# Optimization experiments

Measured on AMD Instinct MI355X. Metric: run time of the kernel, lower is better.

Reference implementation:

```python
import jax, jax.numpy as jnp
import numpy as np

EPS_GN = 1e-8
EPS_ATTN = 1e-8


def setup_inputs() -> dict:
    key = jax.random.key(0)
    ks = jax.random.split(key, 13)
    B, C, N = 4, 512, 2048
    s = 0.02
    return {
        "x": jax.random.normal(ks[0], (B, C, N), jnp.float32),
        "dw_w": jax.random.normal(ks[1], (C, 3), jnp.float32) * s,
        "pw_w": jax.random.normal(ks[2], (C, C), jnp.float32) * s,
        "u_w": jax.random.normal(ks[3], (2 * C, C), jnp.float32) * s,
        "u_b": jax.random.normal(ks[4], (2 * C,), jnp.float32) * s,
        "v_w": jax.random.normal(ks[5], (2 * C, C), jnp.float32) * s,
        "v_b": jax.random.normal(ks[6], (2 * C,), jnp.float32) * s,
        "h_w": jax.random.normal(ks[7], (C, C), jnp.float32) * s,
        "h_b": jax.random.normal(ks[8], (C,), jnp.float32) * s,
        "q_w": jax.random.normal(ks[9], (C, C), jnp.float32) * s,
        "k_w": jax.random.normal(ks[10], (C, C), jnp.float32) * s,
        "o_w": jax.random.normal(ks[11], (C, 2 * C), jnp.float32) * s,
        "o_b": jax.random.normal(ks[12], (C,), jnp.float32) * s,
    }


def reference(x, dw_w, pw_w, u_w, u_b, v_w, v_b, h_w, h_b, q_w, k_w, o_w, o_b):
    # x: [B, C, N]
    C = x.shape[1]
    # GroupNorm(1, C): normalize over (C, N) per sample; affine is identity-init
    # in torch but we follow the module math with default weight=1, bias=0
    mean = jnp.mean(x, axis=(1, 2), keepdims=True)
    var = jnp.var(x, axis=(1, 2), keepdims=True)
    z = (x - mean) * jax.lax.rsqrt(var + EPS_GN)

    # local depthwise conv k=3, pad=1 (cross-correlation), no bias
    zp = jnp.pad(z, ((0, 0), (0, 0), (1, 1)))
    dw = (dw_w[:, 0, None] * zp[:, :, :-2]
          + dw_w[:, 1, None] * zp[:, :, 1:-1]
          + dw_w[:, 2, None] * zp[:, :, 2:])
    # pointwise conv (no bias)
    z = z + jnp.einsum('oc,bcn->bon', pw_w, dw)

    u = jax.nn.sigmoid(jnp.einsum('oc,bcn->bon', u_w, z) + u_b[:, None])  # [B,2C,N]
    v = jnp.einsum('oc,bcn->bon', v_w, z) + v_b[:, None]                  # [B,2C,N]
    h = jnp.einsum('oc,bcn->bno', h_w, z) + h_b                           # [B,N,C]

    q = h @ q_w.T  # [B,N,C]
    k = h @ k_w.T  # [B,N,C]
    scale = 1.0 / jnp.sqrt(jnp.float32(C))

    logits = jnp.einsum('bnc,bmc->bnm', q, k) * scale
    a = jax.nn.relu(logits)
    a = a * a
    a = a / (jnp.sum(a, axis=-1, keepdims=True) + EPS_ATTN)

    av = jnp.einsum('bnm,bom->bon', a, v)  # [B,2C,N]
    y = jnp.einsum('oc,bcn->bon', o_w, u * av) + o_b[:, None]
    return x + y
```

## Files before the change

kernel.cpp:

```cpp
#include <hip/hip_runtime.h>
#include <hip/hip_bf16.h>
#include <cstdint>

typedef __bf16 bhalf;
typedef __bf16 bhalf8 __attribute__((ext_vector_type(8)));
typedef float f32x4 __attribute__((ext_vector_type(4)));

enum { EPI_Z2=0, EPI_UV=1, EPI_BIAS=2, EPI_QK=3, EPI_ATTN=4, EPI_PV=5, EPI_Y=6 };

__device__ __forceinline__ void gl_lds16(const bhalf* g, bhalf* l) {
  __builtin_amdgcn_global_load_lds(
      (const __attribute__((address_space(1))) unsigned int*)g,
      (__attribute__((address_space(3))) unsigned int*)l,
      16, 0, 0);
}
__device__ __forceinline__ void barrier_raw() { asm volatile("s_barrier" ::: "memory"); }
#define VMW(n)  asm volatile("s_waitcnt vmcnt(" #n ")" ::: "memory")
#define LGKM0() asm volatile("s_waitcnt lgkmcnt(0)" ::: "memory")


template<int EPI>
__global__ void __launch_bounds__(512, 2)
gA(const bhalf* __restrict__ A, const bhalf* __restrict__ Bw,
   void* __restrict__ Out, void* __restrict__ Out2,
   const float* __restrict__ bias, const float* __restrict__ bias2,
   int N, int K, long sA, long sB, long sO, long sAuxf, float scale)
{
  constexpr int KSL = 256*64;
  constexpr int REG = 2*KSL;
  constexpr int DBUF = 2*REG;
  __shared__ __align__(16) char lds[2*DBUF];

  const int gx = gridDim.x, gy = gridDim.y;
  const int nwg = gx*gy;
  const int flat = blockIdx.y*gx + blockIdx.x;
  const int q8 = nwg>>3, r8 = nwg&7, xcd = flat&7, o8 = flat>>3;
  const int wsw = (xcd<r8 ? xcd*(q8+1) : r8*(q8+1)+(xcd-r8)*q8) + o8;
  const int bx = wsw % gx, by = wsw / gx;
  const int m0 = by*256, n0 = bx*256;
  const int bz = blockIdx.z;

  const bhalf* Ab = A + (long)bz*sA;
  const bhalf* Bb = Bw + (long)bz*sB;

  const int tid = threadIdx.x, wid = tid>>6, lane = tid&63;
  const int lm = lane&15, kq = lane>>4;
  const int wm = wid>>2, wn = wid&3;
  const int srow = lane>>2;
  const int csw = ((lane&3) ^ ((lane>>3)&3)) * 8;
  const int kqs = kq ^ ((lm>>1)&3);

  f32x4 acc[8][4];
  #pragma unroll
  for (int i=0;i<8;i++)
    #pragma unroll
    for (int j=0;j<4;j++) acc[i][j] = f32x4{0.f,0.f,0.f,0.f};

  auto stageA = [&](int kt){
    char* base = lds + (kt&1)*DBUF;
    const int k0 = kt*64;
    #pragma unroll
    for (int h=0; h<2; h++)
      #pragma unroll
      for (int ksl=0; ksl<2; ksl++){
        bhalf* d = (bhalf*)(base + ksl*KSL + (h*128 + wid*16)*64);
        gl_lds16(Ab + (long)(m0 + h*128 + wid*16 + srow)*K + k0 + ksl*32 + csw, d);
      }
  };
  auto stageB = [&](int kt){
    char* base = lds + (kt&1)*DBUF + REG;
    const int k0 = kt*64;
    #pragma unroll
    for (int h=0; h<2; h++)
      #pragma unroll
      for (int ksl=0; ksl<2; ksl++){
        bhalf* d = (bhalf*)(base + ksl*KSL + (h*128 + wid*16)*64);
        gl_lds16(Bb + (long)(n0 + h*128 + wid*16 + srow)*K + k0 + ksl*32 + csw, d);
      }
  };

  bhalf8 af[4][2], bf[4][2];
  auto readA = [&](int kt, int ih){
    char* base = lds + (kt&1)*DBUF;
    #pragma unroll
    for (int i2=0;i2<4;i2++)
      #pragma unroll
      for (int ksl=0;ksl<2;ksl++)
        af[i2][ksl] = *(const bhalf8*)(base + ksl*KSL + (wm*128 + ih*64 + i2*16 + lm)*64 + kqs*16);
  };
  auto readB = [&](int kt, int jh){
    char* base = lds + (kt&1)*DBUF + REG;
    #pragma unroll
    for (int j2=0;j2<2;j2++)
      #pragma unroll
      for (int ksl=0;ksl<2;ksl++)
        bf[jh*2+j2][ksl] = *(const bhalf8*)(base + ksl*KSL + (wn*64 + jh*32 + j2*16 + lm)*64 + kqs*16);
  };
  auto mfma16 = [&](int ih, int jh){
    __builtin_amdgcn_s_setprio(1);
    #pragma unroll
    for (int i2=0;i2<4;i2++)
      #pragma unroll
      for (int j2=0;j2<2;j2++)
        #pragma unroll
        for (int ksl=0;ksl<2;ksl++)
          acc[ih*4+i2][jh*2+j2] = __builtin_amdgcn_mfma_f32_16x16x32_bf16(
              af[i2][ksl], bf[jh*2+j2][ksl], acc[ih*4+i2][jh*2+j2], 0,0,0);
    __builtin_amdgcn_s_setprio(0);
  };

  const int NT = K>>6;
  stageA(0); stageB(0); stageA(1);
  for (int kt=0; kt<NT; ++kt){
    if (kt==NT-1) { VMW(0); } else { VMW(4); }
    barrier_raw();
    readA(kt,0); readB(kt,0);
    if (kt+1<NT) stageB(kt+1);
    mfma16(0,0);
    barrier_raw();
    readB(kt,1);
    mfma16(0,1);
    barrier_raw();
    readA(kt,1);
    mfma16(1,0);
    barrier_raw();
    if (kt+2<NT) stageA(kt+2);
    mfma16(1,1);
  }
  barrier_raw();

  if constexpr (EPI==EPI_ATTN){
    float rs[8][4];
    #pragma unroll
    for (int i=0;i<8;i++)
      #pragma unroll
      for (int r=0;r<4;r++) rs[i][r]=0.f;
    #pragma unroll
    for (int i=0;i<8;i++){
      #pragma unroll
      for (int j=0;j<4;j++){
        const int lcol = wn*64 + j*16 + lm;
        #pragma unroll
        for (int r=0;r<4;r++){
          const int lrow = wm*128 + i*16 + kq*4 + r;
          float v = acc[i][j][r];
          v *= scale; v = fmaxf(v,0.f); v = v*v;
          rs[i][r] += v;
          const int cb = lcol*2;
          const int lb = lrow*512 + (((cb>>5) ^ ((lrow>>2)&3))<<5) + (cb&31);
          *(bhalf*)(lds + lb) = (bhalf)v;
        }
      }
    }
    float* rd = (float*)Out2;
    #pragma unroll
    for (int i=0;i<8;i++){
      const int rbase = m0 + wm*128 + i*16 + kq*4;
      #pragma unroll
      for (int r=0;r<4;r++){
        float s = rs[i][r];
        s += __shfl_xor(s,1); s += __shfl_xor(s,2);
        s += __shfl_xor(s,4); s += __shfl_xor(s,8);
        if (lm==0) atomicAdd(rd + (long)bz*sAuxf + rbase + r, s);
      }
    }
    LGKM0();
    barrier_raw();
    char* obase = (char*)Out + 2*((long)bz*sO + (long)m0*N + n0);
    const int ldb = N*2;
    #pragma unroll
    for (int it=0; it<16; ++it){
      const int g = (it*512 + tid)*16;
      const int row = g >> 9, off = g & 511;
      const int lb = row*512 + (((off>>5) ^ ((row>>2)&3))<<5) + (off&31);
      uint4 val = *(const uint4*)(lds + lb);
      *(uint4*)(obase + (long)row*ldb + off) = val;
    }
  }
  if constexpr (EPI==EPI_UV){
    const bool uh = n0 < 1024;
    const float* bv = uh ? bias : bias2;
    const int bc0 = uh ? n0 : n0-1024;
    #pragma unroll
    for (int i=0;i<8;i++){
      #pragma unroll
      for (int j=0;j<4;j++){
        const int lcol = wn*64 + j*16 + lm;
        #pragma unroll
        for (int r=0;r<4;r++){
          const int lrow = wm*128 + i*16 + kq*4 + r;
          float v = acc[i][j][r] + bv[bc0 + lcol];
          if (uh){
            v = 1.f/(1.f + __expf(-v));
            const int cb = lcol*2;
            const int lb = lrow*512 + (((cb>>5) ^ ((lrow>>2)&3))<<5) + (cb&31);
            *(bhalf*)(lds + lb) = (bhalf)v;
          } else {
            const int lb = lcol*512 + 2*(lrow ^ ((lcol&15)<<2));
            *(bhalf*)(lds + lb) = (bhalf)v;
          }
        }
      }
    }
    LGKM0();
    barrier_raw();
    if (uh){
      char* obase = (char*)Out + 2*((long)m0*1024 + n0);
      #pragma unroll
      for (int it=0; it<16; ++it){
        const int g = (it*512 + tid)*16;
        const int row = g >> 9, off = g & 511;
        const int lb = row*512 + (((off>>5) ^ ((row>>2)&3))<<5) + (off&31);
        uint4 val = *(const uint4*)(lds + lb);
        *(uint4*)(obase + (long)row*2048 + off) = val;
      }
    } else {
      char* vb = (char*)Out2 + 2*((long)(m0>>11)*1024*2048 + (long)(n0-1024)*2048 + (m0 & 2047));
      #pragma unroll
      for (int it=0; it<16; ++it){
        const int g = (it*512 + tid)*16;
        const int row = g >> 9, off = g & 511;
        const int t0 = off >> 1;
        const int s = (row&15)<<2;
        unsigned long long lo = *(const unsigned long long*)(lds + row*512 + 2*(t0^s));
        unsigned long long hi = *(const unsigned long long*)(lds + row*512 + 2*((t0+4)^s));
        char* dst = vb + (long)row*4096 + off;
        ((unsigned long long*)dst)[0] = lo;
        ((unsigned long long*)dst)[1] = hi;
      }
    }
  }
  (void)scale; (void)bias; (void)bias2; (void)N;
}

template<int EPI>
__global__ void __launch_bounds__(256, 2)
g4k(const bhalf* __restrict__ A, const bhalf* __restrict__ Bw,
    void* __restrict__ Out, void* __restrict__ Out2,
    const float* __restrict__ bias,
    const bhalf* __restrict__ auxb, const float* __restrict__ auxf,
    const float* __restrict__ xadd,
    int M, int N, int K, long sB, int rowshift)
{
  constexpr int KSL = 256*64;
  constexpr int DBUF = 2*KSL;
  __shared__ __align__(16) char lds[2*DBUF];

  const int gx = gridDim.x, gy = gridDim.y;
  const int nwg = gx*gy;
  const int flat = blockIdx.y*gx + blockIdx.x;
  const int q8 = nwg>>3, r8 = nwg&7, xcd = flat&7, o8 = flat>>3;
  const int w = (xcd<r8 ? xcd*(q8+1) : r8*(q8+1)+(xcd-r8)*q8) + o8;
  const int bx = w % gx, by = w / gx;
  const int m0 = by*128, n0 = bx*128;

  const bhalf* Bb = Bw + (rowshift ? (long)(m0>>rowshift)*sB : 0);

  const int tid = threadIdx.x;
  const int wid = tid>>6, lane = tid&63;
  const int lm = lane&15, kq = lane>>4;
  const int wm = wid>>1, wn = wid&1;
  const int srow = lane>>2;
  const int csw = ((lane&3) ^ ((lane>>3)&3))*8;
  const int kqs = kq ^ ((lm>>1)&3);

  f32x4 acc[4][4];
  #pragma unroll
  for (int i=0;i<4;i++)
    #pragma unroll
    for (int j=0;j<4;j++) acc[i][j] = f32x4{0.f,0.f,0.f,0.f};

  auto stage = [&](int kt){
    char* base = lds + (kt&1)*DBUF;
    const int k0 = kt*64;
    #pragma unroll
    for (int c=0;c<4;c++){
      const int r0 = c*64 + wid*16;
      #pragma unroll
      for (int ksl=0; ksl<2; ksl++){
        bhalf* d = (bhalf*)(base + ksl*KSL + r0*64);
        const bhalf* g = (r0 < 128)
          ? A  + (long)(m0 + r0 + srow)*K + k0 + ksl*32 + csw
          : Bb + (long)(n0 + r0 - 128 + srow)*K + k0 + ksl*32 + csw;
        gl_lds16(g, d);
      }
    }
  };

  bhalf8 af[4][2], bf[4][2];
  auto readA = [&](int kt){
    char* base = lds + (kt&1)*DBUF;
    #pragma unroll
    for (int i2=0;i2<4;i2++)
      #pragma unroll
      for (int ksl=0;ksl<2;ksl++)
        af[i2][ksl] = *(const bhalf8*)(base + ksl*KSL + (wm*64 + i2*16 + lm)*64 + kqs*16);
  };
  auto readB = [&](int kt, int jh){
    char* base = lds + (kt&1)*DBUF;
    #pragma unroll
    for (int j2=0;j2<2;j2++)
      #pragma unroll
      for (int ksl=0;ksl<2;ksl++)
        bf[jh*2+j2][ksl] = *(const bhalf8*)(base + ksl*KSL + (128 + wn*64 + jh*32 + j2*16 + lm)*64 + kqs*16);
  };
  auto mfma16 = [&](int jh){
    __builtin_amdgcn_s_setprio(1);
    #pragma unroll
    for (int i2=0;i2<4;i2++)
      #pragma unroll
      for (int j2=0;j2<2;j2++)
        #pragma unroll
        for (int ksl=0;ksl<2;ksl++)
          acc[i2][jh*2+j2] = __builtin_amdgcn_mfma_f32_16x16x32_bf16(
              af[i2][ksl], bf[jh*2+j2][ksl], acc[i2][jh*2+j2], 0,0,0);
    __builtin_amdgcn_s_setprio(0);
  };

  const int NT = K>>6;
  stage(0); stage(1);
  for (int kt=0; kt<NT; ++kt){
    if (kt==NT-1) { VMW(0); } else { VMW(8); }
    barrier_raw();
    readA(kt); readB(kt,0);
    mfma16(0);
    barrier_raw();
    readB(kt,1);
    if (kt+2<NT) stage(kt+2);
    mfma16(1);
  }
  barrier_raw();

  if constexpr (EPI==EPI_Y){
    #pragma unroll
    for (int i=0;i<4;i++){
      #pragma unroll
      for (int j=0;j<4;j++){
        const int lcol = wn*64 + j*16 + lm;
        #pragma unroll
        for (int r=0;r<4;r++){
          const int lrow = wm*64 + i*16 + kq*4 + r;
          float v = acc[i][j][r] + bias[n0 + lcol];
          const int lb = lcol*512 + 4*(lrow ^ ((lcol&15)<<2));
          *(float*)(lds + lb) = v;
        }
      }
    }
    LGKM0();
    barrier_raw();
    const int b = m0 >> 11, nb = m0 & 2047;
    float* ob = (float*)Out + ((long)b*512 + n0)*2048 + nb;
    const float* xb = xadd + ((long)b*512 + n0)*2048 + nb;
    #pragma unroll
    for (int it=0; it<16; ++it){
      const int g = (it*256 + tid)*16;
      const int row = g >> 9, off = g & 511;
      const int t0 = off >> 2;
      const int s = (row&15)<<2;
      f32x4 vv = *(const f32x4*)(lds + row*512 + 4*(t0^s));
      f32x4 xx = *(const f32x4*)(xb + (long)row*2048 + t0);
      *(f32x4*)(ob + (long)row*2048 + t0) = vv + xx;
    }
  } else {
    char* obase; int ldb;
    if constexpr (EPI==EPI_QK){
      bool qh = n0 < 512;
      obase = (char*)(qh?Out:Out2) + 2*((long)m0*512 + (n0 - (qh?0:512)));
      ldb = 1024;
    } else {
      obase = (char*)Out + 2*((long)m0*N + n0);
      ldb = N*2;
    }
    #pragma unroll
    for (int i=0;i<4;i++){
      #pragma unroll
      for (int j=0;j<4;j++){
        const int lcol = wn*64 + j*16 + lm;
        #pragma unroll
        for (int r=0;r<4;r++){
          const int lrow = wm*64 + i*16 + kq*4 + r;
          float v = acc[i][j][r];
          if constexpr (EPI==EPI_Z2)
            v += (float)auxb[(long)(m0+lrow)*N + n0 + lcol];
          if constexpr (EPI==EPI_BIAS)
            v += bias[n0 + lcol];
          if constexpr (EPI==EPI_PV){
            const int rowg = m0 + lrow;
            float den = auxf[rowg];
            v *= __builtin_amdgcn_rcpf(den + 1e-8f);
            v *= (float)auxb[(long)rowg*1024 + n0 + lcol];
          }
          const int cb = lcol*2;
          const int lb = lrow*256 + (((cb>>5) ^ ((lrow>>2)&3))<<5) + (cb&31);
          *(bhalf*)(lds + lb) = (bhalf)v;
        }
      }
    }
    LGKM0();
    barrier_raw();
    #pragma unroll
    for (int it=0; it<8; ++it){
      const int g = (it*256 + tid)*16;
      const int row = g >> 8, off = g & 255;
      const int lb = row*256 + (((off>>5) ^ ((row>>2)&3))<<5) + (off&31);
      uint4 val = *(const uint4*)(lds + lb);
      *(uint4*)(obase + (long)row*ldb + off) = val;
    }
  }
  (void)M; (void)xadd; (void)bias; (void)auxb; (void)auxf;
}

struct CvtArgs { const float* src[7]; bhalf* dst[7]; int n[7]; };
__global__ void cvt_multi(CvtArgs a) {
  int seg = blockIdx.y;
  int i = (blockIdx.x*256 + threadIdx.x)*4;
  if (i >= a.n[seg]) return;
  float4 f = *(const float4*)(a.src[seg] + i);
  bhalf* d = a.dst[seg] + i;
  d[0]=(bhalf)f.x; d[1]=(bhalf)f.y; d[2]=(bhalf)f.z; d[3]=(bhalf)f.w;
}

__global__ void gn_part(const float* __restrict__ x, float* __restrict__ ps, float* __restrict__ pss) {
  int b = blockIdx.y;
  const float* xb = x + (long)b*(512*2048);
  float s=0.f, ss=0.f;
  #pragma unroll
  for (int it=0; it<8; it++){
    int idx = ((it*128 + blockIdx.x)*256 + threadIdx.x)*4;
    float4 f = *(const float4*)(xb + idx);
    s  += f.x+f.y+f.z+f.w;
    ss += f.x*f.x+f.y*f.y+f.z*f.z+f.w*f.w;
  }
  for (int off=32; off; off>>=1){ s += __shfl_xor(s,off); ss += __shfl_xor(ss,off); }
  __shared__ float ls[4], lss[4];
  int wid = threadIdx.x>>6, lane = threadIdx.x&63;
  if (lane==0){ ls[wid]=s; lss[wid]=ss; }
  __syncthreads();
  if (threadIdx.x==0){
    s = ls[0]+ls[1]+ls[2]+ls[3]; ss = lss[0]+lss[1]+lss[2]+lss[3];
    ps[b*128 + blockIdx.x] = s; pss[b*128 + blockIdx.x] = ss;
  }
}

__global__ void gn_final(const float* __restrict__ ps, const float* __restrict__ pss,
                         float* __restrict__ stats) {
  int b = blockIdx.x;
  float s = ps[b*128 + threadIdx.x], ss = pss[b*128 + threadIdx.x];
  for (int off=32; off; off>>=1){ s += __shfl_xor(s,off); ss += __shfl_xor(ss,off); }
  __shared__ float l0[2], l1[2];
  int wid = threadIdx.x>>6, lane = threadIdx.x&63;
  if (lane==0){ l0[wid]=s; l1[wid]=ss; }
  __syncthreads();
  if (threadIdx.x==0){
    s = l0[0]+l0[1]; ss = l1[0]+l1[1];
    float mean = s*(1.f/1048576.f);
    float var  = ss*(1.f/1048576.f) - mean*mean;
    stats[b*2] = mean; stats[b*2+1] = rsqrtf(var + 1e-8f);
  }
}

__global__ void norm_dw_T(const float* __restrict__ x, const float* __restrict__ stats,
                          const float* __restrict__ dw_w,
                          bhalf* __restrict__ zT, bhalf* __restrict__ dwT) {
  int b = blockIdx.z, n0 = blockIdx.x*32, c0 = blockIdx.y*32;
  float mean = stats[b*2], rstd = stats[b*2+1];
  __shared__ float zs[32][35];
  int tx = threadIdx.x, ty = threadIdx.y;
  #pragma unroll
  for (int r=0;r<4;r++){
    int c = c0 + ty + r*8;
    for (int cc=tx; cc<34; cc+=32){
      int n = n0 - 1 + cc;
      float v = 0.f;
      if (n>=0 && n<2048) v = (x[((long)b*512 + c)*2048 + n] - mean)*rstd;
      zs[ty + r*8][cc] = v;
    }
  }
  __syncthreads();
  float w0 = dw_w[(c0+tx)*3+0], w1 = dw_w[(c0+tx)*3+1], w2 = dw_w[(c0+tx)*3+2];
  #pragma unroll
  for (int r=0;r<4;r++){
    int ln = ty + r*8;
    float z = zs[tx][ln+1];
    float d = w0*zs[tx][ln] + w1*zs[tx][ln+1] + w2*zs[tx][ln+2];
    long o = ((long)b*2048 + n0 + ln)*512 + c0 + tx;
    zT[o] = (bhalf)z; dwT[o] = (bhalf)d;
  }
}

extern "C" void kernel_launch(void* const* d_in, const int* in_sizes, int n_in,
                              void* d_out, int out_size, void* d_ws, size_t ws_size,
                              hipStream_t stream) {
  (void)in_sizes; (void)n_in; (void)out_size; (void)ws_size;
  const float* x    = (const float*)d_in[0];
  const float* dw_w = (const float*)d_in[1];
  const float* pw_w = (const float*)d_in[2];
  const float* u_w  = (const float*)d_in[3];
  const float* u_b  = (const float*)d_in[4];
  const float* v_w  = (const float*)d_in[5];
  const float* v_b  = (const float*)d_in[6];
  const float* h_w  = (const float*)d_in[7];
  const float* h_b  = (const float*)d_in[8];
  const float* q_w  = (const float*)d_in[9];
  const float* k_w  = (const float*)d_in[10];
  const float* o_w  = (const float*)d_in[11];
  const float* o_b  = (const float*)d_in[12];
  float* out = (float*)d_out;

  char* ws = (char*)d_ws;
  size_t off = 0;
  auto alloc = [&](size_t bytes) -> void* {
    void* p = ws + off; off = (off + bytes + 255) & ~(size_t)255; return p;
  };

  float* ps    = (float*)alloc(4*128*4);
  float* pss   = (float*)alloc(4*128*4);
  float* stats = (float*)alloc(4*2*4);
  float* rden  = (float*)alloc(4*2048*4);
  bhalf* wb_pw = (bhalf*)alloc(512*512*2);
  bhalf* wb_uv = (bhalf*)alloc((size_t)2048*512*2);
  bhalf* wb_h  = (bhalf*)alloc(512*512*2);
  bhalf* wb_qk = (bhalf*)alloc((size_t)1024*512*2);
  bhalf* wb_o  = (bhalf*)alloc((size_t)512*1024*2);
  const size_t ACT = (size_t)4*2048*512;
  bhalf* zT   = (bhalf*)alloc(ACT*2);
  bhalf* dwT  = (bhalf*)alloc(ACT*2);
  bhalf* z2T  = (bhalf*)alloc(ACT*2);
  bhalf* ub   = (bhalf*)alloc(ACT*2*2);
  bhalf* v_fm = (bhalf*)alloc(ACT*2*2);
  bhalf* hb   = (bhalf*)alloc(ACT*2);
  bhalf* wsc  = (bhalf*)alloc((size_t)4*2048*2048*2);
  bhalf* uav  = (bhalf*)alloc(ACT*2*2);
  bhalf* qb = zT;  bhalf* kb = dwT;

  hipMemsetAsync(rden, 0, 4*2048*4, stream);

  CvtArgs ca;
  ca.src[0]=pw_w; ca.dst[0]=wb_pw;           ca.n[0]=512*512;
  ca.src[1]=u_w;  ca.dst[1]=wb_uv;           ca.n[1]=1024*512;
  ca.src[2]=v_w;  ca.dst[2]=wb_uv+1024*512;  ca.n[2]=1024*512;
  ca.src[3]=h_w;  ca.dst[3]=wb_h;            ca.n[3]=512*512;
  ca.src[4]=q_w;  ca.dst[4]=wb_qk;           ca.n[4]=512*512;
  ca.src[5]=k_w;  ca.dst[5]=wb_qk+512*512;   ca.n[5]=512*512;
  ca.src[6]=o_w;  ca.dst[6]=wb_o;            ca.n[6]=512*1024;
  cvt_multi<<<dim3(512,7), 256, 0, stream>>>(ca);

  gn_part<<<dim3(128,4), 256, 0, stream>>>(x, ps, pss);
  gn_final<<<dim3(4), 128, 0, stream>>>(ps, pss, stats);

  norm_dw_T<<<dim3(64,16,4), dim3(32,8), 0, stream>>>(x, stats, dw_w, zT, dwT);

  const float iscl = 0.044194173824159216f;
  g4k<EPI_Z2><<<dim3(4,64,1), 256, 0, stream>>>(dwT, wb_pw, z2T, nullptr,
      nullptr, zT, nullptr, nullptr, 8192, 512, 512, 0, 0);
  gA<EPI_UV><<<dim3(8,32,1), 512, 0, stream>>>(z2T, wb_uv, ub, v_fm,
      u_b, v_b, 2048, 512, 0, 0, 0, 0, 0.f);
  g4k<EPI_BIAS><<<dim3(4,64,1), 256, 0, stream>>>(z2T, wb_h, hb, nullptr,
      h_b, nullptr, nullptr, nullptr, 8192, 512, 512, 0, 0);
  g4k<EPI_QK><<<dim3(8,64,1), 256, 0, stream>>>(hb, wb_qk, qb, kb,
      nullptr, nullptr, nullptr, nullptr, 8192, 1024, 512, 0, 0);
  gA<EPI_ATTN><<<dim3(8,8,4), 512, 0, stream>>>(qb, kb, wsc, rden,
      nullptr, nullptr, 2048, 512,
      (long)2048*512, (long)2048*512, (long)2048*2048, 2048, iscl);
  g4k<EPI_PV><<<dim3(8,64,1), 256, 0, stream>>>(wsc, v_fm, uav, nullptr,
      nullptr, ub, rden, nullptr, 8192, 1024, 2048, (long)1024*2048, 11);
  g4k<EPI_Y><<<dim3(4,64,1), 256, 0, stream>>>(uav, wb_o, out, nullptr,
      o_b, nullptr, nullptr, x, 8192, 512, 1024, 0, 0);
}
```

Baseline: 183.4 us.

## Replace 256x256 gA kernel with 128x128 g4k tiles for UV and attention GEMMs

Removes the 512-thread 256x256-tile GEMM kernel and routes the UV projection and QK^T attention-score GEMMs through the existing 256-thread 128x128-tile kernel. The g4k kernel gains batch strides, a second bias, a scale parameter, and ported ATTN/UV epilogues. Smaller tiles give four times as many workgroups (1024 instead of 256), which improves occupancy and load balance across CUs. The cost is less operand reuse per tile, so more global and LDS traffic per FLOP.

Measured after the change: 191.8 us. +4.6%, slower.

```diff
diff --git a/kernel.cpp b/kernel.cpp
--- a/kernel.cpp
+++ b/kernel.cpp
@@ -20,227 +20,13 @@
 
 
 template<int EPI>
-__global__ void __launch_bounds__(512, 2)
-gA(const bhalf* __restrict__ A, const bhalf* __restrict__ Bw,
-   void* __restrict__ Out, void* __restrict__ Out2,
-   const float* __restrict__ bias, const float* __restrict__ bias2,
-   int N, int K, long sA, long sB, long sO, long sAuxf, float scale)
-{
-  constexpr int KSL = 256*64;
-  constexpr int REG = 2*KSL;
-  constexpr int DBUF = 2*REG;
-  __shared__ __align__(16) char lds[2*DBUF];
-
-  const int gx = gridDim.x, gy = gridDim.y;
-  const int nwg = gx*gy;
-  const int flat = blockIdx.y*gx + blockIdx.x;
-  const int q8 = nwg>>3, r8 = nwg&7, xcd = flat&7, o8 = flat>>3;
-  const int wsw = (xcd<r8 ? xcd*(q8+1) : r8*(q8+1)+(xcd-r8)*q8) + o8;
-  const int bx = wsw % gx, by = wsw / gx;
-  const int m0 = by*256, n0 = bx*256;
-  const int bz = blockIdx.z;
-
-  const bhalf* Ab = A + (long)bz*sA;
-  const bhalf* Bb = Bw + (long)bz*sB;
-
-  const int tid = threadIdx.x, wid = tid>>6, lane = tid&63;
-  const int lm = lane&15, kq = lane>>4;
-  const int wm = wid>>2, wn = wid&3;
-  const int srow = lane>>2;
-  const int csw = ((lane&3) ^ ((lane>>3)&3)) * 8;
-  const int kqs = kq ^ ((lm>>1)&3);
-
-  f32x4 acc[8][4];
-  #pragma unroll
-  for (int i=0;i<8;i++)
-    #pragma unroll
-    for (int j=0;j<4;j++) acc[i][j] = f32x4{0.f,0.f,0.f,0.f};
-
-  auto stageA = [&](int kt){
-    char* base = lds + (kt&1)*DBUF;
-    const int k0 = kt*64;
-    #pragma unroll
-    for (int h=0; h<2; h++)
-      #pragma unroll
-      for (int ksl=0; ksl<2; ksl++){
-        bhalf* d = (bhalf*)(base + ksl*KSL + (h*128 + wid*16)*64);
-        gl_lds16(Ab + (long)(m0 + h*128 + wid*16 + srow)*K + k0 + ksl*32 + csw, d);
-      }
-  };
-  auto stageB = [&](int kt){
-    char* base = lds + (kt&1)*DBUF + REG;
-    const int k0 = kt*64;
-    #pragma unroll
-    for (int h=0; h<2; h++)
-      #pragma unroll
-      for (int ksl=0; ksl<2; ksl++){
-        bhalf* d = (bhalf*)(base + ksl*KSL + (h*128 + wid*16)*64);
-        gl_lds16(Bb + (long)(n0 + h*128 + wid*16 + srow)*K + k0 + ksl*32 + csw, d);
-      }
-  };
-
-  bhalf8 af[4][2], bf[4][2];
-  auto readA = [&](int kt, int ih){
-    char* base = lds + (kt&1)*DBUF;
-    #pragma unroll
-    for (int i2=0;i2<4;i2++)
-      #pragma unroll
-      for (int ksl=0;ksl<2;ksl++)
-        af[i2][ksl] = *(const bhalf8*)(base + ksl*KSL + (wm*128 + ih*64 + i2*16 + lm)*64 + kqs*16);
-  };
-  auto readB = [&](int kt, int jh){
-    char* base = lds + (kt&1)*DBUF + REG;
-    #pragma unroll
-    for (int j2=0;j2<2;j2++)
-      #pragma unroll
-      for (int ksl=0;ksl<2;ksl++)
-        bf[jh*2+j2][ksl] = *(const bhalf8*)(base + ksl*KSL + (wn*64 + jh*32 + j2*16 + lm)*64 + kqs*16);
-  };
-  auto mfma16 = [&](int ih, int jh){
-    __builtin_amdgcn_s_setprio(1);
-    #pragma unroll
-    for (int i2=0;i2<4;i2++)
-      #pragma unroll
-      for (int j2=0;j2<2;j2++)
-        #pragma unroll
-        for (int ksl=0;ksl<2;ksl++)
-          acc[ih*4+i2][jh*2+j2] = __builtin_amdgcn_mfma_f32_16x16x32_bf16(
-              af[i2][ksl], bf[jh*2+j2][ksl], acc[ih*4+i2][jh*2+j2], 0,0,0);
-    __builtin_amdgcn_s_setprio(0);
-  };
-
-  const int NT = K>>6;
-  stageA(0); stageB(0); stageA(1);
-  for (int kt=0; kt<NT; ++kt){
-    if (kt==NT-1) { VMW(0); } else { VMW(4); }
-    barrier_raw();
-    readA(kt,0); readB(kt,0);
-    if (kt+1<NT) stageB(kt+1);
-    mfma16(0,0);
-    barrier_raw();
-    readB(kt,1);
-    mfma16(0,1);
-    barrier_raw();
-    readA(kt,1);
-    mfma16(1,0);
-    barrier_raw();
-    if (kt+2<NT) stageA(kt+2);
-    mfma16(1,1);
-  }
-  barrier_raw();
-
-  if constexpr (EPI==EPI_ATTN){
-    float rs[8][4];
-    #pragma unroll
-    for (int i=0;i<8;i++)
-      #pragma unroll
-      for (int r=0;r<4;r++) rs[i][r]=0.f;
-    #pragma unroll
-    for (int i=0;i<8;i++){
-      #pragma unroll
-      for (int j=0;j<4;j++){
-        const int lcol = wn*64 + j*16 + lm;
-        #pragma unroll
-        for (int r=0;r<4;r++){
-          const int lrow = wm*128 + i*16 + kq*4 + r;
-          float v = acc[i][j][r];
-          v *= scale; v = fmaxf(v,0.f); v = v*v;
-          rs[i][r] += v;
-          const int cb = lcol*2;
-          const int lb = lrow*512 + (((cb>>5) ^ ((lrow>>2)&3))<<5) + (cb&31);
-          *(bhalf*)(lds + lb) = (bhalf)v;
-        }
-      }
-    }
-    float* rd = (float*)Out2;
-    #pragma unroll
-    for (int i=0;i<8;i++){
-      const int rbase = m0 + wm*128 + i*16 + kq*4;
-      #pragma unroll
-      for (int r=0;r<4;r++){
-        float s = rs[i][r];
-        s += __shfl_xor(s,1); s += __shfl_xor(s,2);
-        s += __shfl_xor(s,4); s += __shfl_xor(s,8);
-        if (lm==0) atomicAdd(rd + (long)bz*sAuxf + rbase + r, s);
-      }
-    }
-    LGKM0();
-    barrier_raw();
-    char* obase = (char*)Out + 2*((long)bz*sO + (long)m0*N + n0);
-    const int ldb = N*2;
-    #pragma unroll
-    for (int it=0; it<16; ++it){
-      const int g = (it*512 + tid)*16;
-      const int row = g >> 9, off = g & 511;
-      const int lb = row*512 + (((off>>5) ^ ((row>>2)&3))<<5) + (off&31);
-      uint4 val = *(const uint4*)(lds + lb);
-      *(uint4*)(obase + (long)row*ldb + off) = val;
-    }
-  }
-  if constexpr (EPI==EPI_UV){
-    const bool uh = n0 < 1024;
-    const float* bv = uh ? bias : bias2;
-    const int bc0 = uh ? n0 : n0-1024;
-    #pragma unroll
-    for (int i=0;i<8;i++){
-      #pragma unroll
-      for (int j=0;j<4;j++){
-        const int lcol = wn*64 + j*16 + lm;
-        #pragma unroll
-        for (int r=0;r<4;r++){
-          const int lrow = wm*128 + i*16 + kq*4 + r;
-          float v = acc[i][j][r] + bv[bc0 + lcol];
-          if (uh){
-            v = 1.f/(1.f + __expf(-v));
-            const int cb = lcol*2;
-            const int lb = lrow*512 + (((cb>>5) ^ ((lrow>>2)&3))<<5) + (cb&31);
-            *(bhalf*)(lds + lb) = (bhalf)v;
-          } else {
-            const int lb = lcol*512 + 2*(lrow ^ ((lcol&15)<<2));
-            *(bhalf*)(lds + lb) = (bhalf)v;
-          }
-        }
-      }
-    }
-    LGKM0();
-    barrier_raw();
-    if (uh){
-      char* obase = (char*)Out + 2*((long)m0*1024 + n0);
-      #pragma unroll
-      for (int it=0; it<16; ++it){
-        const int g = (it*512 + tid)*16;
-        const int row = g >> 9, off = g & 511;
-        const int lb = row*512 + (((off>>5) ^ ((row>>2)&3))<<5) + (off&31);
-        uint4 val = *(const uint4*)(lds + lb);
-        *(uint4*)(obase + (long)row*2048 + off) = val;
-      }
-    } else {
-      char* vb = (char*)Out2 + 2*((long)(m0>>11)*1024*2048 + (long)(n0-1024)*2048 + (m0 & 2047));
-      #pragma unroll
-      for (int it=0; it<16; ++it){
-        const int g = (it*512 + tid)*16;
-        const int row = g >> 9, off = g & 511;
-        const int t0 = off >> 1;
-        const int s = (row&15)<<2;
-        unsigned long long lo = *(const unsigned long long*)(lds + row*512 + 2*(t0^s));
-        unsigned long long hi = *(const unsigned long long*)(lds + row*512 + 2*((t0+4)^s));
-        char* dst = vb + (long)row*4096 + off;
-        ((unsigned long long*)dst)[0] = lo;
-        ((unsigned long long*)dst)[1] = hi;
-      }
-    }
-  }
-  (void)scale; (void)bias; (void)bias2; (void)N;
-}
-
-template<int EPI>
 __global__ void __launch_bounds__(256, 2)
 g4k(const bhalf* __restrict__ A, const bhalf* __restrict__ Bw,
     void* __restrict__ Out, void* __restrict__ Out2,
-    const float* __restrict__ bias,
+    const float* __restrict__ bias, const float* __restrict__ bias2,
     const bhalf* __restrict__ auxb, const float* __restrict__ auxf,
     const float* __restrict__ xadd,
-    int M, int N, int K, long sB, int rowshift)
+    int N, int K, long sA, long sB, long sO, float scale, int rowshift)
 {
   constexpr int KSL = 256*64;
   constexpr int DBUF = 2*KSL;
@@ -253,8 +39,10 @@
   const int w = (xcd<r8 ? xcd*(q8+1) : r8*(q8+1)+(xcd-r8)*q8) + o8;
   const int bx = w % gx, by = w / gx;
   const int m0 = by*128, n0 = bx*128;
-
-  const bhalf* Bb = Bw + (rowshift ? (long)(m0>>rowshift)*sB : 0);
+  const int bz = blockIdx.z;
+
+  const bhalf* Ab = A + (long)bz*sA;
+  const bhalf* Bb = Bw + (long)bz*sB + (rowshift ? (long)(m0>>rowshift)*sB : 0);
 
   const int tid = threadIdx.x;
   const int wid = tid>>6, lane = tid&63;
@@ -280,7 +68,7 @@
       for (int ksl=0; ksl<2; ksl++){
         bhalf* d = (bhalf*)(base + ksl*KSL + r0*64);
         const bhalf* g = (r0 < 128)
-          ? A  + (long)(m0 + r0 + srow)*K + k0 + ksl*32 + csw
+          ? Ab + (long)(m0 + r0 + srow)*K + k0 + ksl*32 + csw
           : Bb + (long)(n0 + r0 - 128 + srow)*K + k0 + ksl*32 + csw;
         gl_lds16(g, d);
       }
@@ -360,6 +148,105 @@
       f32x4 vv = *(const f32x4*)(lds + row*512 + 4*(t0^s));
       f32x4 xx = *(const f32x4*)(xb + (long)row*2048 + t0);
       *(f32x4*)(ob + (long)row*2048 + t0) = vv + xx;
+    }
+  } else if constexpr (EPI==EPI_ATTN){
+    float rs[4][4];
+    #pragma unroll
+    for (int i=0;i<4;i++)
+      #pragma unroll
+      for (int r=0;r<4;r++) rs[i][r]=0.f;
+    #pragma unroll
+    for (int i=0;i<4;i++){
+      #pragma unroll
+      for (int j=0;j<4;j++){
+        const int lcol = wn*64 + j*16 + lm;
+        #pragma unroll
+        for (int r=0;r<4;r++){
+          const int lrow = wm*64 + i*16 + kq*4 + r;
+          float v = acc[i][j][r];
+          v *= scale; v = fmaxf(v,0.f); v = v*v;
+          rs[i][r] += v;
+          const int cb = lcol*2;
+          const int lb = lrow*256 + (((cb>>5) ^ ((lrow>>2)&3))<<5) + (cb&31);
+          *(bhalf*)(lds + lb) = (bhalf)v;
+        }
+      }
+    }
+    float* rd = (float*)Out2 + (long)bz*2048;
+    #pragma unroll
+    for (int i=0;i<4;i++){
+      const int rbase = m0 + wm*64 + i*16 + kq*4;
+      #pragma unroll
+      for (int r=0;r<4;r++){
+        float s = rs[i][r];
+        s += __shfl_xor(s,1); s += __shfl_xor(s,2);
+        s += __shfl_xor(s,4); s += __shfl_xor(s,8);
+        if (lm==0) atomicAdd(rd + rbase + r, s);
+      }
+    }
+    LGKM0();
+    barrier_raw();
+    char* obase = (char*)Out + 2*((long)bz*sO + (long)m0*N + n0);
+    const int ldb = N*2;
+    #pragma unroll
+    for (int it=0; it<8; ++it){
+      const int g = (it*256 + tid)*16;
+      const int row = g >> 8, off = g & 255;
+      const int lb = row*256 + (((off>>5) ^ ((row>>2)&3))<<5) + (off&31);
+      uint4 val = *(const uint4*)(lds + lb);
+      *(uint4*)(obase + (long)row*ldb + off) = val;
+    }
+  } else if constexpr (EPI==EPI_UV){
+    const bool uh = n0 < 1024;
+    const float* bv = uh ? bias : bias2;
+    const int bc0 = uh ? n0 : n0-1024;
+    #pragma unroll
+    for (int i=0;i<4;i++){
+      #pragma unroll
+      for (int j=0;j<4;j++){
+        const int lcol = wn*64 + j*16 + lm;
+        #pragma unroll
+        for (int r=0;r<4;r++){
+          const int lrow = wm*64 + i*16 + kq*4 + r;
+          float v = acc[i][j][r] + bv[bc0 + lcol];
+          if (uh){
+            v = 1.f/(1.f + __expf(-v));
+            const int cb = lcol*2;
+            const int lb = lrow*256 + (((cb>>5) ^ ((lrow>>2)&3))<<5) + (cb&31);
+            *(bhalf*)(lds + lb) = (bhalf)v;
+          } else {
+            const int lb = lcol*256 + 2*(lrow ^ ((lcol&15)<<2));
+            *(bhalf*)(lds + lb) = (bhalf)v;
+          }
+        }
+      }
+    }
+    LGKM0();
+    barrier_raw();
+    if (uh){
+      char* obase = (char*)Out + 2*((long)m0*1024 + n0);
+      #pragma unroll
+      for (int it=0; it<8; ++it){
+        const int g = (it*256 + tid)*16;
+        const int row = g >> 8, off = g & 255;
+        const int lb = row*256 + (((off>>5) ^ ((row>>2)&3))<<5) + (off&31);
+        uint4 val = *(const uint4*)(lds + lb);
+        *(uint4*)(obase + (long)row*2048 + off) = val;
+      }
+    } else {
+      char* vb = (char*)Out2 + 2*((long)(m0>>11)*1024*2048 + (long)(n0-1024)*2048 + (m0 & 2047));
+      #pragma unroll
+      for (int it=0; it<8; ++it){
+        const int g = (it*256 + tid)*16;
+        const int row = g >> 8, off = g & 255;
+        const int t0 = off >> 1;
+        const int s = (row&15)<<2;
+        unsigned long long lo = *(const unsigned long long*)(lds + row*256 + 2*(t0^s));
+        unsigned long long hi = *(const unsigned long long*)(lds + row*256 + 2*((t0+4)^s));
+        char* dst = vb + (long)row*4096 + off;
+        ((unsigned long long*)dst)[0] = lo;
+        ((unsigned long long*)dst)[1] = hi;
+      }
     }
   } else {
     char* obase; int ldb;
@@ -407,7 +294,7 @@
       *(uint4*)(obase + (long)row*ldb + off) = val;
     }
   }
-  (void)M; (void)xadd; (void)bias; (void)auxb; (void)auxf;
+  (void)xadd; (void)bias; (void)bias2; (void)auxb; (void)auxf; (void)scale;
 }
 
 struct CvtArgs { const float* src[7]; bhalf* dst[7]; int n[7]; };
@@ -552,18 +439,19 @@
 
   const float iscl = 0.044194173824159216f;
   g4k<EPI_Z2><<<dim3(4,64,1), 256, 0, stream>>>(dwT, wb_pw, z2T, nullptr,
-      nullptr, zT, nullptr, nullptr, 8192, 512, 512, 0, 0);
-  gA<EPI_UV><<<dim3(8,32,1), 512, 0, stream>>>(z2T, wb_uv, ub, v_fm,
-      u_b, v_b, 2048, 512, 0, 0, 0, 0, 0.f);
+      nullptr, nullptr, zT, nullptr, nullptr, 512, 512, 0,0,0, 0.f, 0);
+  g4k<EPI_UV><<<dim3(16,64,1), 256, 0, stream>>>(z2T, wb_uv, ub, v_fm,
+      u_b, v_b, nullptr, nullptr, nullptr, 2048, 512, 0,0,0, 0.f, 0);
   g4k<EPI_BIAS><<<dim3(4,64,1), 256, 0, stream>>>(z2T, wb_h, hb, nullptr,
-      h_b, nullptr, nullptr, nullptr, 8192, 512, 512, 0, 0);
+      h_b, nullptr, nullptr, nullptr, nullptr, 512, 512, 0,0,0, 0.f, 0);
   g4k<EPI_QK><<<dim3(8,64,1), 256, 0, stream>>>(hb, wb_qk, qb, kb,
-      nullptr, nullptr, nullptr, nullptr, 8192, 1024, 512, 0, 0);
-  gA<EPI_ATTN><<<dim3(8,8,4), 512, 0, stream>>>(qb, kb, wsc, rden,
-      nullptr, nullptr, 2048, 512,
-      (long)2048*512, (long)2048*512, (long)2048*2048, 2048, iscl);
+      nullptr, nullptr, nullptr, nullptr, nullptr, 1024, 512, 0,0,0, 0.f, 0);
+  g4k<EPI_ATTN><<<dim3(16,16,4), 256, 0, stream>>>(qb, kb, wsc, rden,
+      nullptr, nullptr, nullptr, nullptr, nullptr, 2048, 512,
+      (long)2048*512, (long)2048*512, (long)2048*2048, iscl, 0);
   g4k<EPI_PV><<<dim3(8,64,1), 256, 0, stream>>>(wsc, v_fm, uav, nullptr,
-      nullptr, ub, rden, nullptr, 8192, 1024, 2048, (long)1024*2048, 11);
+      nullptr, nullptr, ub, rden, nullptr, 1024, 2048,
+      0, (long)1024*2048, 0, 0.f, 11);
   g4k<EPI_Y><<<dim3(4,64,1), 256, 0, stream>>>(uav, wb_o, out, nullptr,
-      o_b, nullptr, nullptr, x, 8192, 512, 1024, 0, 0);
-}
+      o_b, nullptr, nullptr, nullptr, x, 512, 1024, 0,0,0, 0.f, 0);
+}
```

## Fold h projection into q/k weights to drop one GEMM

Applied to the files above, without the earlier changes.

Precomputes combined weights Wq·Wh and Wk·Wh (plus the bias term Wqk·h_b) at runtime, so q and k come straight from z2 in a single GEMM. This removes the separate h GEMM and the write and read of the h activation. In exchange it adds a small transpose, a weight-product GEMM and a bias-reduction kernel each call, and changes bf16 rounding because h is no longer rounded to bf16 before the q/k projection. It relies on an EPI_ST epilogue in g4k that the diff does not define, so the store path for the weight product is assumed to fall through to the default.

After: 185.7 us. Within noise of the previous version (+1.3%).

```diff
diff --git a/kernel.cpp b/kernel.cpp
--- a/kernel.cpp
+++ b/kernel.cpp
@@ -6,7 +6,7 @@
 typedef __bf16 bhalf8 __attribute__((ext_vector_type(8)));
 typedef float f32x4 __attribute__((ext_vector_type(4)));
 
-enum { EPI_Z2=0, EPI_UV=1, EPI_BIAS=2, EPI_QK=3, EPI_ATTN=4, EPI_PV=5, EPI_Y=6 };
+enum { EPI_Z2=0, EPI_UV=1, EPI_BIAS=2, EPI_QK=3, EPI_ATTN=4, EPI_PV=5, EPI_Y=6, EPI_ST=7 };
 
 __device__ __forceinline__ void gl_lds16(const bhalf* g, bhalf* l) {
   __builtin_amdgcn_global_load_lds(
@@ -384,6 +384,8 @@
             v += (float)auxb[(long)(m0+lrow)*N + n0 + lcol];
           if constexpr (EPI==EPI_BIAS)
             v += bias[n0 + lcol];
+          if constexpr (EPI==EPI_QK)
+            v += bias[n0 + lcol];
           if constexpr (EPI==EPI_PV){
             const int rowg = m0 + lrow;
             float den = auxf[rowg];
@@ -418,6 +420,32 @@
   float4 f = *(const float4*)(a.src[seg] + i);
   bhalf* d = a.dst[seg] + i;
   d[0]=(bhalf)f.x; d[1]=(bhalf)f.y; d[2]=(bhalf)f.z; d[3]=(bhalf)f.w;
+}
+
+__global__ void transpose_bf16(const bhalf* __restrict__ in, bhalf* __restrict__ out,
+                               int R, int C) {
+  __shared__ bhalf t[32][33];
+  int r0 = blockIdx.x*32, c0 = blockIdx.y*32;
+  int tx = threadIdx.x, ty = threadIdx.y;
+  #pragma unroll
+  for (int r=0;r<4;r++)
+    t[ty + r*8][tx] = in[(long)(r0 + ty + r*8)*C + c0 + tx];
+  __syncthreads();
+  #pragma unroll
+  for (int r=0;r<4;r++)
+    out[(long)(c0 + ty + r*8)*R + r0 + tx] = t[tx][ty + r*8];
+}
+
+__global__ void qk_bias(const bhalf* __restrict__ wqk, const float* __restrict__ hb,
+                        float* __restrict__ bq){
+  int row = blockIdx.x*4 + (threadIdx.x>>6);
+  int lane = threadIdx.x & 63;
+  const bhalf* p = wqk + (long)row*512;
+  float s = 0.f;
+  #pragma unroll
+  for (int j=0;j<8;j++) s += (float)p[lane*8+j] * hb[lane*8+j];
+  for (int off=32; off; off>>=1) s += __shfl_xor(s, off);
+  if (lane==0) bq[row] = s;
 }
 
 __global__ void gn_part(const float* __restrict__ x, float* __restrict__ ps, float* __restrict__ pss) {
@@ -517,10 +545,13 @@
   float* pss   = (float*)alloc(4*128*4);
   float* stats = (float*)alloc(4*2*4);
   float* rden  = (float*)alloc(4*2048*4);
+  float* bq    = (float*)alloc(1024*4);
   bhalf* wb_pw = (bhalf*)alloc(512*512*2);
   bhalf* wb_uv = (bhalf*)alloc((size_t)2048*512*2);
   bhalf* wb_h  = (bhalf*)alloc(512*512*2);
+  bhalf* hwT   = (bhalf*)alloc(512*512*2);
   bhalf* wb_qk = (bhalf*)alloc((size_t)1024*512*2);
+  bhalf* wqk2  = (bhalf*)alloc((size_t)1024*512*2);
   bhalf* wb_o  = (bhalf*)alloc((size_t)512*1024*2);
   const size_t ACT = (size_t)4*2048*512;
   bhalf* zT   = (bhalf*)alloc(ACT*2);
@@ -528,7 +559,6 @@
   bhalf* z2T  = (bhalf*)alloc(ACT*2);
   bhalf* ub   = (bhalf*)alloc(ACT*2*2);
   bhalf* v_fm = (bhalf*)alloc(ACT*2*2);
-  bhalf* hb   = (bhalf*)alloc(ACT*2);
   bhalf* wsc  = (bhalf*)alloc((size_t)4*2048*2048*2);
   bhalf* uav  = (bhalf*)alloc(ACT*2*2);
   bhalf* qb = zT;  bhalf* kb = dwT;
@@ -545,6 +575,11 @@
   ca.src[6]=o_w;  ca.dst[6]=wb_o;            ca.n[6]=512*1024;
   cvt_multi<<<dim3(512,7), 256, 0, stream>>>(ca);
 
+  transpose_bf16<<<dim3(16,16), dim3(32,8), 0, stream>>>(wb_h, hwT, 512, 512);
+  g4k<EPI_ST><<<dim3(4,8,1), 256, 0, stream>>>(wb_qk, hwT, wqk2, nullptr,
+      nullptr, nullptr, nullptr, nullptr, 1024, 512, 512, 0, 0);
+  qk_bias<<<dim3(256), 256, 0, stream>>>(wb_qk, h_b, bq);
+
   gn_part<<<dim3(128,4), 256, 0, stream>>>(x, ps, pss);
   gn_final<<<dim3(4), 128, 0, stream>>>(ps, pss, stats);
 
@@ -555,10 +590,8 @@
       nullptr, zT, nullptr, nullptr, 8192, 512, 512, 0, 0);
   gA<EPI_UV><<<dim3(8,32,1), 512, 0, stream>>>(z2T, wb_uv, ub, v_fm,
       u_b, v_b, 2048, 512, 0, 0, 0, 0, 0.f);
-  g4k<EPI_BIAS><<<dim3(4,64,1), 256, 0, stream>>>(z2T, wb_h, hb, nullptr,
-      h_b, nullptr, nullptr, nullptr, 8192, 512, 512, 0, 0);
-  g4k<EPI_QK><<<dim3(8,64,1), 256, 0, stream>>>(hb, wb_qk, qb, kb,
-      nullptr, nullptr, nullptr, nullptr, 8192, 1024, 512, 0, 0);
+  g4k<EPI_QK><<<dim3(8,64,1), 256, 0, stream>>>(z2T, wqk2, qb, kb,
+      bq, nullptr, nullptr, nullptr, 8192, 1024, 512, 0, 0);
   gA<EPI_ATTN><<<dim3(8,8,4), 512, 0, stream>>>(qb, kb, wsc, rden,
       nullptr, nullptr, 2048, 512,
       (long)2048*512, (long)2048*512, (long)2048*2048, 2048, iscl);
```
